# Kernel tuning notes

Measured on AMD Instinct MI355X. Metric: run time of the kernel, lower is better.

## Reference

```python
import jax, jax.numpy as jnp
import numpy as np

COORD_DIM = 2
ENTITY_DIM = 1024
FIELD_DIM = 512
INPUT_DIM = 512
NUM_ENTITIES = 512
FIELD_RESOLUTION = 10000  # grid_size = 100


def _gelu(x):
    return jax.nn.gelu(x, approximate=False)  # torch nn.GELU default (erf)


def setup_inputs() -> dict:
    key = jax.random.key(0)
    ks = jax.random.split(key, 9)
    std = 0.02  # matches _init_parameters
    B, S = 8, 4096
    x = jax.random.normal(ks[0], (B, S, INPUT_DIM), dtype=jnp.float32)
    # DensityField: density_projection = Linear(D,F) GELU Linear(F,F) GELU; coordinate_generator = Linear(F,2)
    W1 = jax.random.normal(ks[1], (INPUT_DIM, FIELD_DIM), jnp.float32) * std
    b1 = jnp.zeros((FIELD_DIM,), jnp.float32)
    W2 = jax.random.normal(ks[2], (FIELD_DIM, FIELD_DIM), jnp.float32) * std
    b2 = jnp.zeros((FIELD_DIM,), jnp.float32)
    Wc = jax.random.normal(ks[3], (FIELD_DIM, COORD_DIM), jnp.float32) * std
    bc = jnp.zeros((COORD_DIM,), jnp.float32)
    # entity_mapper: Linear(F+2, F) GELU Linear(F, E+2+1)
    We1 = jax.random.normal(ks[4], (FIELD_DIM + COORD_DIM, FIELD_DIM), jnp.float32) * std
    be1 = jnp.zeros((FIELD_DIM,), jnp.float32)
    We2 = jax.random.normal(ks[5], (FIELD_DIM, ENTITY_DIM + COORD_DIM + 1), jnp.float32) * std
    be2 = jnp.zeros((ENTITY_DIM + COORD_DIM + 1,), jnp.float32)
    # output_projection: Linear(E, 2E) GELU Linear(2E, D)
    Wo1 = jax.random.normal(ks[6], (ENTITY_DIM, 2 * ENTITY_DIM), jnp.float32) * std
    bo1 = jnp.zeros((2 * ENTITY_DIM,), jnp.float32)
    Wo2 = jax.random.normal(ks[7], (2 * ENTITY_DIM, INPUT_DIM), jnp.float32) * std
    bo2 = jnp.zeros((INPUT_DIM,), jnp.float32)
    return dict(x=x, W1=W1, b1=b1, W2=W2, b2=b2, Wc=Wc, bc=bc,
                We1=We1, be1=be1, We2=We2, be2=be2,
                Wo1=Wo1, bo1=bo1, Wo2=Wo2, bo2=bo2)


def _forward(x, W1, b1, W2, b2, Wc, bc, We1, be1, We2, be2, Wo1, bo1, Wo2, bo2):
    # --- DensityField ---
    df = _gelu(_gelu(x @ W1 + b1) @ W2 + b2)          # [B,S,F]
    coords = df @ Wc + bc                              # [B,S,2]
    # --- ContinuousEntityExtractor ---
    field_input = jnp.concatenate([coords, df], axis=-1)          # [B,S,2+F]
    ef = _gelu(field_input @ We1 + be1) @ We2 + be2                # [B,S,E+3]
    importance = jnp.linalg.norm(ef, axis=-1)                      # [B,S]
    _, top_idx = jax.lax.top_k(importance, NUM_ENTITIES)           # [B,Ne]
    sel = jnp.take_along_axis(ef, top_idx[..., None], axis=1)     # [B,Ne,E+3]
    positions = sel[..., :COORD_DIM]                               # [B,Ne,2]
    states = sel[..., COORD_DIM:COORD_DIM + ENTITY_DIM]            # [B,Ne,E]
    # --- ContinuousOutputGenerator ---
    proj = _gelu(states @ Wo1 + bo1) @ Wo2 + bo2                   # [B,Ne,D]
    grid_size = int(FIELD_RESOLUTION ** 0.5)
    g = jnp.linspace(-1.0, 1.0, grid_size)
    gx, gy = jnp.meshgrid(g, g, indexing='ij')
    grid = jnp.stack([gx.ravel(), gy.ravel()], axis=-1)            # [G2,2]
    # squared euclidean distances via expansion (torch: cdist then **2)
    g2 = jnp.sum(grid * grid, axis=-1)                             # [G2]
    p2 = jnp.sum(positions * positions, axis=-1)                   # [B,Ne]
    gp = jnp.einsum('gc,bnc->bgn', grid, positions)                # [B,G2,Ne]
    sq = g2[None, :, None] + p2[:, None, :] - 2.0 * gp             # [B,G2,Ne]
    attn = jnp.exp(-sq / 0.1)
    attn = attn / (attn.sum(axis=-1, keepdims=True) + 1e-8)
    out = jnp.einsum('bgn,bnd->bgd', attn, proj)                   # [B,G2,D]
    return out


def reference(x, W1, b1, W2, b2, Wc, bc, We1, be1, We2, be2, Wo1, bo1, Wo2, bo2):
    return _forward(x, W1, b1, W2, b2, Wc, bc, We1, be1, We2, be2, Wo1, bo1, Wo2, bo2)
```

## Files before the change

### kernel.cpp

```cpp
#include <hip/hip_runtime.h>
#include <hip/hip_bf16.h>
#include <math.h>


typedef __attribute__((ext_vector_type(8))) short bf16x8;
typedef __attribute__((ext_vector_type(4))) float f32x4;

__device__ __forceinline__ float gelu_exact(float x) {
    return 0.5f * x * (1.0f + erff(x * 0.7071067811865476f));
}

__device__ __forceinline__ void async_copy16(const void* g, void* l) {
    __builtin_amdgcn_global_load_lds(
        (const __attribute__((address_space(1))) unsigned int*)g,
        (__attribute__((address_space(3))) unsigned int*)l, 16, 0, 0);
}

__global__ __launch_bounds__(256) void split_kernel(
    const float* __restrict__ in,
    __hip_bfloat16* __restrict__ hi, __hip_bfloat16* __restrict__ lo)
{
    const int i4 = blockIdx.x * 256 + threadIdx.x;
    const float4 v = ((const float4*)in)[i4];
    __hip_bfloat16 h0 = __float2bfloat16(v.x);
    __hip_bfloat16 h1 = __float2bfloat16(v.y);
    __hip_bfloat16 h2 = __float2bfloat16(v.z);
    __hip_bfloat16 h3 = __float2bfloat16(v.w);
    __hip_bfloat16 l0 = __float2bfloat16(v.x - __bfloat162float(h0));
    __hip_bfloat16 l1 = __float2bfloat16(v.y - __bfloat162float(h1));
    __hip_bfloat16 l2 = __float2bfloat16(v.z - __bfloat162float(h2));
    __hip_bfloat16 l3 = __float2bfloat16(v.w - __bfloat162float(h3));
    union { __hip_bfloat16 h[4]; short4 s; } uh, ul;
    uh.h[0] = h0; uh.h[1] = h1; uh.h[2] = h2; uh.h[3] = h3;
    ul.h[0] = l0; ul.h[1] = l1; ul.h[2] = l2; ul.h[3] = l3;
    ((short4*)hi)[i4] = uh.s;
    ((short4*)lo)[i4] = ul.s;
}

__global__ __launch_bounds__(256) void transpose_split_kernel(
    const float* __restrict__ in,
    __hip_bfloat16* __restrict__ outH, __hip_bfloat16* __restrict__ outL,
    int K, int N)
{
    __shared__ float tile[32][33];
    const int k0 = blockIdx.y * 32, n0 = blockIdx.x * 32;
    const int t = threadIdx.x;
    const int lr = t >> 5, lc = t & 31;
    #pragma unroll
    for (int p = 0; p < 4; p++) {
        const int r = p * 8 + lr;
        const int n = n0 + lc;
        tile[r][lc] = (n < N) ? in[(size_t)(k0 + r) * N + n] : 0.f;
    }
    __syncthreads();
    #pragma unroll
    for (int p = 0; p < 4; p++) {
        const int r = p * 8 + lr;
        const float v = tile[lc][r];
        const __hip_bfloat16 h = __float2bfloat16(v);
        const __hip_bfloat16 l = __float2bfloat16(v - __bfloat162float(h));
        outH[(size_t)(n0 + r) * K + k0 + lc] = h;
        outL[(size_t)(n0 + r) * K + k0 + lc] = l;
    }
}

__global__ __launch_bounds__(256) void init_kernel(
    float* __restrict__ IMP, float* __restrict__ CRD,
    const float* __restrict__ bc)
{
    const int t = blockIdx.x * 256 + threadIdx.x;
    IMP[t] = 0.f;
    ((float2*)CRD)[t] = make_float2(bc[0], bc[1]);
}

template<bool GELU, bool RANK2, bool EFMODE, bool FUSEC>
__global__ __launch_bounds__(256, 2) void gemm3k(
    const __hip_bfloat16* __restrict__ Ahi, const __hip_bfloat16* __restrict__ Alo,
    const __hip_bfloat16* __restrict__ Bhi, const __hip_bfloat16* __restrict__ Blo,
    const float* __restrict__ bias,
    __hip_bfloat16* __restrict__ Chi, __hip_bfloat16* __restrict__ Clo,
    __hip_bfloat16* __restrict__ EFB, float* __restrict__ EFC,
    float* __restrict__ IMP,
    const float* __restrict__ A2, const float* __restrict__ W2r,
    float* __restrict__ CRD, const float* __restrict__ Wc)
{
    __shared__ __align__(16) __hip_bfloat16 AsH[2][4096];
    __shared__ __align__(16) __hip_bfloat16 AsL[2][4096];
    __shared__ __align__(16) __hip_bfloat16 BsH[2][4096];
    __shared__ __align__(16) __hip_bfloat16 BsL[2][4096];
    const int t = threadIdx.x;
    const int wave = t >> 6, lane = t & 63;
    const int wave_m = wave >> 1, wave_n = wave & 1;
    const int fr = lane & 15, quad = lane >> 4;
    const int gx = gridDim.x;
    const int nwg = gx * gridDim.y;
    int lid = blockIdx.y * gx + blockIdx.x;
    {
        const int chunk = nwg >> 3;
        lid = (lid & 7) * chunk + (lid >> 3);
    }
    const int m0 = (lid / gx) * 128;
    const int n0 = (lid % gx) * 128;
    const int lrow   = lane & 15;
    const int lchunk = (lane >> 4) * 8;

    f32x4 acc[4][4] = {};

    auto STAGE = [&](int buf, int step) {
        const int kk = step << 5;
        #pragma unroll
        for (int s = 0; s < 2; s++) {
            const int seg = wave * 2 + s;
            const size_t ao = (size_t)(m0 + seg * 16 + lrow) * 512 + kk + lchunk;
            const size_t bo = (size_t)(n0 + seg * 16 + lrow) * 512 + kk + lchunk;
            async_copy16(Ahi + ao, &AsH[buf][seg * 512]);
            async_copy16(Alo + ao, &AsL[buf][seg * 512]);
            async_copy16(Bhi + bo, &BsH[buf][seg * 512]);
            async_copy16(Blo + bo, &BsL[buf][seg * 512]);
        }
    };

    STAGE(0, 0);
    __syncthreads();
    int cur = 0;
    const int abase = wave_m * 2048 + quad * 128 + fr * 8;
    const int bbase = wave_n * 2048 + quad * 128 + fr * 8;
    for (int step = 0; step < 16; ++step) {
        if (step + 1 < 16) STAGE(cur ^ 1, step + 1);
        bf16x8 ah[4], al[4], bh[4], bl[4];
        #pragma unroll
        for (int i = 0; i < 4; i++) {
            ah[i] = *(const bf16x8*)&AsH[cur][abase + i * 512];
            al[i] = *(const bf16x8*)&AsL[cur][abase + i * 512];
        }
        #pragma unroll
        for (int j = 0; j < 4; j++) {
            bh[j] = *(const bf16x8*)&BsH[cur][bbase + j * 512];
            bl[j] = *(const bf16x8*)&BsL[cur][bbase + j * 512];
        }
        __builtin_amdgcn_s_setprio(1);
        #pragma unroll
        for (int i = 0; i < 4; i++)
            #pragma unroll
            for (int j = 0; j < 4; j++)
                acc[i][j] = __builtin_amdgcn_mfma_f32_16x16x32_bf16(
                    ah[i], bh[j], acc[i][j], 0, 0, 0);
        #pragma unroll
        for (int i = 0; i < 4; i++)
            #pragma unroll
            for (int j = 0; j < 4; j++)
                acc[i][j] = __builtin_amdgcn_mfma_f32_16x16x32_bf16(
                    ah[i], bl[j], acc[i][j], 0, 0, 0);
        #pragma unroll
        for (int i = 0; i < 4; i++)
            #pragma unroll
            for (int j = 0; j < 4; j++)
                acc[i][j] = __builtin_amdgcn_mfma_f32_16x16x32_bf16(
                    al[i], bh[j], acc[i][j], 0, 0, 0);
        __builtin_amdgcn_s_setprio(0);
        __syncthreads();
        cur ^= 1;
    }

    #pragma unroll
    for (int i = 0; i < 4; i++) {
        const int gmb = m0 + wave_m * 64 + i * 16 + quad * 4;
        float a2x[4], a2y[4];
        if (RANK2) {
            #pragma unroll
            for (int r = 0; r < 4; r++) {
                a2x[r] = A2[(size_t)(gmb + r) * 2];
                a2y[r] = A2[(size_t)(gmb + r) * 2 + 1];
            }
        }
        float f0[4] = {0.f, 0.f, 0.f, 0.f};
        float f1[4] = {0.f, 0.f, 0.f, 0.f};
        #pragma unroll
        for (int j = 0; j < 4; j++) {
            const int gn = n0 + wave_n * 64 + j * 16 + fr;
            const bool nok = !EFMODE || (gn < 1027);
            const float bv = nok ? bias[gn] : 0.f;
            float w2a = 0.f, w2b = 0.f;
            if (RANK2) { w2a = W2r[gn]; w2b = W2r[512 + gn]; }
            float wcx = 0.f, wcy = 0.f;
            if (FUSEC) {
                const float2 wc = ((const float2*)Wc)[gn];
                wcx = wc.x; wcy = wc.y;
            }
            #pragma unroll
            for (int r = 0; r < 4; r++) {
                const int gm = gmb + r;
                float v = acc[i][j][r] + bv;
                if (RANK2) v += a2x[r] * w2a + a2y[r] * w2b;
                if (GELU) v = gelu_exact(v);
                if (EFMODE) {
                    if (gn < 2) EFC[(size_t)gm * 2 + gn] = v;
                    else if (gn < 1026)
                        EFB[(size_t)gm * 1024 + gn - 2] = __float2bfloat16(v);
                    if (nok) f0[r] += v * v;
                } else {
                    const __hip_bfloat16 h = __float2bfloat16(v);
                    const __hip_bfloat16 l =
                        __float2bfloat16(v - __bfloat162float(h));
                    Chi[(size_t)gm * 512 + gn] = h;
                    Clo[(size_t)gm * 512 + gn] = l;
                    if (FUSEC) { f0[r] += v * wcx; f1[r] += v * wcy; }
                }
            }
        }
        if (EFMODE || FUSEC) {
            #pragma unroll
            for (int r = 0; r < 4; r++) {
                float a = f0[r], b = f1[r];
                #pragma unroll
                for (int off = 1; off < 16; off <<= 1) {
                    a += __shfl_xor(a, off);
                    if (FUSEC) b += __shfl_xor(b, off);
                }
                if (fr == 0) {
                    if (FUSEC) {
                        atomicAdd(&CRD[(size_t)(gmb + r) * 2],     a);
                        atomicAdd(&CRD[(size_t)(gmb + r) * 2 + 1], b);
                    } else {
                        atomicAdd(&IMP[gmb + r], a);
                    }
                }
            }
        }
    }
}

__global__ __launch_bounds__(1024) void topk_kernel(
    const float* __restrict__ IMP, int* __restrict__ IDX)
{
    __shared__ float v[4096];
    __shared__ int   ix[4096];
    const int b = blockIdx.x, t = threadIdx.x;
    for (int i = t; i < 4096; i += 1024) {
        v[i] = sqrtf(IMP[b * 4096 + i]);
        ix[i] = i;
    }
    __syncthreads();
    for (int k = 2; k <= 4096; k <<= 1) {
        for (int j = k >> 1; j > 0; j >>= 1) {
            for (int q = 0; q < 4; q++) {
                const int i = t + (q << 10);
                const int l = i ^ j;
                if (l > i) {
                    const float vi = v[i], vl = v[l];
                    const int   ii = ix[i], il = ix[l];
                    const bool after = (vi < vl) || (vi == vl && ii > il);
                    const bool dirAsc = ((i & k) == 0);
                    if (dirAsc ? after : !after) {
                        v[i] = vl; v[l] = vi; ix[i] = il; ix[l] = ii;
                    }
                }
            }
            __syncthreads();
        }
    }
    if (t < 512) IDX[b * 512 + t] = ix[t];
}

__global__ __launch_bounds__(256) void gather_kernel(
    const __hip_bfloat16* __restrict__ EFB, const float* __restrict__ EFC,
    const int* __restrict__ IDX,
    float* __restrict__ POS, __hip_bfloat16* __restrict__ ST)
{
    const int bn  = blockIdx.x;
    const int b   = bn >> 9;
    const int row = IDX[bn];
    const size_t src = (size_t)(b * 4096) + row;
    const int t = threadIdx.x;
    if (t < 2) POS[(size_t)bn * 2 + t] = EFC[src * 2 + t];
    const unsigned int* s = (const unsigned int*)(EFB + src * 1024);
    unsigned int* d = (unsigned int*)(ST + (size_t)bn * 1024);
    d[t]       = s[t];
    d[t + 256] = s[t + 256];
}

__global__ __launch_bounds__(256) void transpose_cvt_kernel(
    const float* __restrict__ in, __hip_bfloat16* __restrict__ out,
    int K, int N)
{
    __shared__ float tile[32][33];
    const int k0 = blockIdx.y * 32, n0 = blockIdx.x * 32;
    const int t = threadIdx.x;
    const int lr = t >> 5, lc = t & 31;
    #pragma unroll
    for (int p = 0; p < 4; p++) {
        const int r = p * 8 + lr;
        tile[r][lc] = in[(size_t)(k0 + r) * N + n0 + lc];
    }
    __syncthreads();
    #pragma unroll
    for (int p = 0; p < 4; p++) {
        const int r = p * 8 + lr;
        out[(size_t)(n0 + r) * K + k0 + lc] = __float2bfloat16(tile[lc][r]);
    }
}

__global__ __launch_bounds__(256) void transpose_proj_kernel(
    const __hip_bfloat16* __restrict__ in, __hip_bfloat16* __restrict__ out)
{
    __shared__ __hip_bfloat16 tile[32][33];
    const int b = blockIdx.z;
    const int n0 = blockIdx.y * 32, d0 = blockIdx.x * 32;
    const int t = threadIdx.x;
    const int lr = t >> 5, lc = t & 31;
    #pragma unroll
    for (int p = 0; p < 4; p++) {
        const int r = p * 8 + lr;
        tile[r][lc] = in[((size_t)b * 512 + n0 + r) * 512 + d0 + lc];
    }
    __syncthreads();
    #pragma unroll
    for (int p = 0; p < 4; p++) {
        const int r = p * 8 + lr;
        out[((size_t)b * 512 + d0 + r) * 512 + n0 + lc] = tile[lc][r];
    }
}

template<bool GELU>
__global__ __launch_bounds__(256, 4) void gemm_post(
    const __hip_bfloat16* __restrict__ A,
    const __hip_bfloat16* __restrict__ BT,
    const float* __restrict__ bias,
    __hip_bfloat16* __restrict__ C,
    int N, int K)
{
    __shared__ __align__(16) __hip_bfloat16 As[2][4096];
    __shared__ __align__(16) __hip_bfloat16 Bs[2][4096];
    const int t = threadIdx.x;
    const int wave = t >> 6, lane = t & 63;
    const int wave_m = wave >> 1, wave_n = wave & 1;
    const int fr = lane & 15, quad = lane >> 4;
    const int gx = gridDim.x;
    const int nwg = gx * gridDim.y;
    int lid = blockIdx.y * gx + blockIdx.x;
    {
        const int chunk = nwg >> 3;
        lid = (lid & 7) * chunk + (lid >> 3);
    }
    const int m0 = (lid / gx) * 128;
    const int n0 = (lid % gx) * 128;
    const int lrow   = lane & 15;
    const int lchunk = (lane >> 4) * 8;
    const int nsteps = K >> 5;

    f32x4 acc[4][4] = {};

    auto STAGE = [&](int buf, int step) {
        const int kk = step << 5;
        #pragma unroll
        for (int s = 0; s < 2; s++) {
            const int seg = wave * 2 + s;
            async_copy16(A  + (size_t)(m0 + seg * 16 + lrow) * K + kk + lchunk,
                         &As[buf][seg * 512]);
            async_copy16(BT + (size_t)(n0 + seg * 16 + lrow) * K + kk + lchunk,
                         &Bs[buf][seg * 512]);
        }
    };

    STAGE(0, 0);
    __syncthreads();
    int cur = 0;
    const int abase = wave_m * 2048 + quad * 128 + fr * 8;
    const int bbase = wave_n * 2048 + quad * 128 + fr * 8;
    for (int step = 0; step < nsteps; ++step) {
        if (step + 1 < nsteps) STAGE(cur ^ 1, step + 1);
        bf16x8 af[4], bfv[4];
        #pragma unroll
        for (int i = 0; i < 4; i++)
            af[i] = *(const bf16x8*)&As[cur][abase + i * 512];
        #pragma unroll
        for (int j = 0; j < 4; j++)
            bfv[j] = *(const bf16x8*)&Bs[cur][bbase + j * 512];
        __builtin_amdgcn_s_setprio(1);
        #pragma unroll
        for (int i = 0; i < 4; i++)
            #pragma unroll
            for (int j = 0; j < 4; j++)
                acc[i][j] = __builtin_amdgcn_mfma_f32_16x16x32_bf16(
                    af[i], bfv[j], acc[i][j], 0, 0, 0);
        __builtin_amdgcn_s_setprio(0);
        __syncthreads();
        cur ^= 1;
    }
    #pragma unroll
    for (int i = 0; i < 4; i++) {
        const int gm = m0 + wave_m * 64 + i * 16 + quad * 4;
        #pragma unroll
        for (int j = 0; j < 4; j++) {
            const int gn = n0 + wave_n * 64 + j * 16 + fr;
            const float bv = bias[gn];
            #pragma unroll
            for (int r = 0; r < 4; r++) {
                float v = acc[i][j][r] + bv;
                if (GELU) v = gelu_exact(v);
                C[(size_t)(gm + r) * N + gn] = __float2bfloat16(v);
            }
        }
    }
}

__global__ __launch_bounds__(256) void attn_mfma_kernel(
    const float* __restrict__ POS,
    const __hip_bfloat16* __restrict__ PROJT,
    float* __restrict__ OUT)
{
    __shared__ __align__(16) __hip_bfloat16 Bs[2][8192];
    __shared__ float2 pos_s[512];
    __shared__ float srow_s[4][16];
    const int t = threadIdx.x;
    const int wave = t >> 6, lane = t & 63;
    const int fr = lane & 15, quad = lane >> 4;
    const int b  = blockIdx.z;
    const int g0 = blockIdx.x * 64;
    const int d0 = blockIdx.y * 256;
    const int lrow   = lane & 15;
    const int lchunk = (lane >> 4) * 8;

    {
        const float2* p = (const float2*)(POS + (size_t)b * 512 * 2);
        pos_s[t]       = p[t];
        pos_s[256 + t] = p[256 + t];
    }
    const int g = g0 + wave * 16 + fr;
    const bool gv = g < 10000;
    const float step = 2.0f / 99.0f;
    const int gi = gv ? (g / 100) : 0;
    const int gj = gv ? (g - gi * 100) : 0;
    const float gx = -1.f + step * (float)gi;
    const float gy = -1.f + step * (float)gj;

    auto STAGE = [&](int buf, int n0s) {
        #pragma unroll
        for (int s = 0; s < 4; s++) {
            const int seg = wave * 4 + s;
            const __hip_bfloat16* gB = PROJT
                + ((size_t)b * 512 + d0 + seg * 16 + lrow) * 512
                + n0s + lchunk;
            async_copy16(gB, &Bs[buf][seg * 512]);
        }
    };

    f32x4 acc[16] = {};
    float wsum = 0.f;
    STAGE(0, 0);
    __syncthreads();
    int cur = 0;
    const int bbase = quad * 128 + fr * 8;

    for (int it = 0; it < 16; ++it) {
        const int n0 = it * 32;
        if (it + 1 < 16) STAGE(cur ^ 1, (it + 1) * 32);
        bf16x8 wf;
        float wl = 0.f;
        #pragma unroll
        for (int j = 0; j < 8; j++) {
            const int n = n0 + quad * 8 + j;
            const float2 pn = pos_s[n];
            const float dx = gx - pn.x, dy = gy - pn.y;
            const float w = gv ? __expf(-10.0f * (dx * dx + dy * dy)) : 0.f;
            const __hip_bfloat16 wb = __float2bfloat16(w);
            union { __hip_bfloat16 h; short s; } u; u.h = wb;
            wf[j] = u.s;
            wl += __bfloat162float(wb);
        }
        wsum += wl;
        __builtin_amdgcn_s_setprio(1);
        #pragma unroll
        for (int j = 0; j < 16; j++) {
            const bf16x8 bv = *(const bf16x8*)&Bs[cur][j * 512 + bbase];
            acc[j] = __builtin_amdgcn_mfma_f32_16x16x32_bf16(wf, bv, acc[j], 0, 0, 0);
        }
        __builtin_amdgcn_s_setprio(0);
        __syncthreads();
        cur ^= 1;
    }
    wsum += __shfl_xor(wsum, 16);
    wsum += __shfl_xor(wsum, 32);
    if (lane < 16) srow_s[wave][lane] = wsum;
    __syncthreads();
    const int rbase = quad * 4;
    float inv[4];
    #pragma unroll
    for (int r = 0; r < 4; r++)
        inv[r] = 1.0f / (srow_s[wave][rbase + r] + 1e-8f);
    #pragma unroll
    for (int j = 0; j < 16; j++) {
        const int col = d0 + j * 16 + fr;
        #pragma unroll
        for (int r = 0; r < 4; r++) {
            const int gr = g0 + wave * 16 + rbase + r;
            if (gr < 10000)
                OUT[((size_t)b * 10000 + gr) * 512 + col] = acc[j][r] * inv[r];
        }
    }
}

extern "C" void kernel_launch(void* const* d_in, const int* in_sizes, int n_in,
                              void* d_out, int out_size, void* d_ws, size_t ws_size,
                              hipStream_t stream)
{
    const float* x   = (const float*)d_in[0];
    const float* W1  = (const float*)d_in[1];
    const float* b1  = (const float*)d_in[2];
    const float* W2  = (const float*)d_in[3];
    const float* b2  = (const float*)d_in[4];
    const float* Wc  = (const float*)d_in[5];
    const float* bc  = (const float*)d_in[6];
    const float* We1 = (const float*)d_in[7];
    const float* be1 = (const float*)d_in[8];
    const float* We2 = (const float*)d_in[9];
    const float* be2 = (const float*)d_in[10];
    const float* Wo1 = (const float*)d_in[11];
    const float* bo1 = (const float*)d_in[12];
    const float* Wo2 = (const float*)d_in[13];
    const float* bo2 = (const float*)d_in[14];
    float* out = (float*)d_out;

    const size_t BS = 32768;
    const size_t ACT = BS * 512;
    __hip_bfloat16* P0h = (__hip_bfloat16*)d_ws;
    __hip_bfloat16* P0l = P0h + ACT;
    __hip_bfloat16* P1h = P0l + ACT;
    __hip_bfloat16* P1l = P1h + ACT;
    __hip_bfloat16* EFB = P1l + ACT;
    float* EFC = (float*)(EFB + BS * 1024);
    float* CRD = EFC + BS * 2;
    float* IMP = CRD + BS * 2;
    int*   IDX = (int*)(IMP + BS);
    float* POS = (float*)(IDX + 4096);
    __hip_bfloat16* W1Th = (__hip_bfloat16*)(POS + 4096 * 2);
    __hip_bfloat16* W1Tl = W1Th + 512 * 512;
    __hip_bfloat16* W2Th = W1Tl + 512 * 512;
    __hip_bfloat16* W2Tl = W2Th + 512 * 512;
    __hip_bfloat16* We1Th = W2Tl + 512 * 512;
    __hip_bfloat16* We1Tl = We1Th + 512 * 512;
    __hip_bfloat16* We2Th = We1Tl + 512 * 512;
    __hip_bfloat16* We2Tl = We2Th + (size_t)1152 * 512;
    __hip_bfloat16* ST    = P0h;
    __hip_bfloat16* H4    = ST + (size_t)4096 * 1024;
    __hip_bfloat16* PROJ  = H4 + (size_t)4096 * 2048;
    __hip_bfloat16* PROJT = PROJ + (size_t)4096 * 512;
    __hip_bfloat16* Wo1T  = PROJT + (size_t)4096 * 512;
    __hip_bfloat16* Wo2T  = Wo1T + (size_t)2048 * 1024;

    dim3 blk(256);
    split_kernel<<<dim3(16384), blk, 0, stream>>>(x, P0h, P0l);
    transpose_split_kernel<<<dim3(16, 16), blk, 0, stream>>>(W1, W1Th, W1Tl, 512, 512);
    transpose_split_kernel<<<dim3(16, 16), blk, 0, stream>>>(W2, W2Th, W2Tl, 512, 512);
    transpose_split_kernel<<<dim3(16, 16), blk, 0, stream>>>(We1 + 2 * 512, We1Th, We1Tl, 512, 512);
    transpose_split_kernel<<<dim3(36, 16), blk, 0, stream>>>(We2, We2Th, We2Tl, 512, 1027);
    init_kernel<<<dim3(128), blk, 0, stream>>>(IMP, CRD, bc);
    gemm3k<true, false, false, false><<<dim3(4, 256), blk, 0, stream>>>(
        P0h, P0l, W1Th, W1Tl, b1, P1h, P1l,
        nullptr, nullptr, nullptr, nullptr, nullptr, nullptr, nullptr);
    gemm3k<true, false, false, true><<<dim3(4, 256), blk, 0, stream>>>(
        P1h, P1l, W2Th, W2Tl, b2, P0h, P0l,
        nullptr, nullptr, nullptr, nullptr, nullptr, CRD, Wc);
    gemm3k<true, true, false, false><<<dim3(4, 256), blk, 0, stream>>>(
        P0h, P0l, We1Th, We1Tl, be1, P1h, P1l,
        nullptr, nullptr, nullptr, CRD, We1, nullptr, nullptr);
    gemm3k<false, false, true, false><<<dim3(9, 256), blk, 0, stream>>>(
        P1h, P1l, We2Th, We2Tl, be2, nullptr, nullptr,
        EFB, EFC, IMP, nullptr, nullptr, nullptr, nullptr);
    topk_kernel<<<dim3(8), dim3(1024), 0, stream>>>(IMP, IDX);
    transpose_cvt_kernel<<<dim3(64, 32), blk, 0, stream>>>(Wo1, Wo1T, 1024, 2048);
    transpose_cvt_kernel<<<dim3(16, 64), blk, 0, stream>>>(Wo2, Wo2T, 2048, 512);
    gather_kernel<<<dim3(4096), blk, 0, stream>>>(EFB, EFC, IDX, POS, ST);
    gemm_post<true><<<dim3(16, 32), blk, 0, stream>>>(
        ST, Wo1T, bo1, H4, 2048, 1024);
    gemm_post<false><<<dim3(4, 32), blk, 0, stream>>>(
        H4, Wo2T, bo2, PROJ, 512, 2048);
    transpose_proj_kernel<<<dim3(16, 16, 8), blk, 0, stream>>>(PROJ, PROJT);
    attn_mfma_kernel<<<dim3(157, 2, 8), blk, 0, stream>>>(POS, PROJT, out);
}
```

Baseline: 976.0 us.

## Load split-bf16 GEMM fragments directly from global and simplify LDS staging

The split-precision gemm3k drops LDS staging and instead loads MFMA fragments straight from global memory into registers. Two register sets are ping-ponged so the next K-step's loads are in flight while the current MFMAs run, and the XCD tile remapping is reworked. gemm_post and the attention kernel change their LDS layout to row-major [rows][32] with a different lane-to-address mapping and drop s_setprio. The attention kernel also goes from double to single buffering with an extra barrier. This trades LDS traffic and barriers for uncoalesced, cache-dependent global loads, and it loses the copy/compute overlap in the attention kernel.

```diff
diff --git a/kernel.cpp b/kernel.cpp
--- a/kernel.cpp
+++ b/kernel.cpp
@@ -84,83 +84,69 @@
     const float* __restrict__ A2, const float* __restrict__ W2r,
     float* __restrict__ CRD, const float* __restrict__ Wc)
 {
-    __shared__ __align__(16) __hip_bfloat16 AsH[2][4096];
-    __shared__ __align__(16) __hip_bfloat16 AsL[2][4096];
-    __shared__ __align__(16) __hip_bfloat16 BsH[2][4096];
-    __shared__ __align__(16) __hip_bfloat16 BsL[2][4096];
     const int t = threadIdx.x;
     const int wave = t >> 6, lane = t & 63;
     const int wave_m = wave >> 1, wave_n = wave & 1;
     const int fr = lane & 15, quad = lane >> 4;
     const int gx = gridDim.x;
-    const int nwg = gx * gridDim.y;
-    int lid = blockIdx.y * gx + blockIdx.x;
-    {
-        const int chunk = nwg >> 3;
-        lid = (lid & 7) * chunk + (lid >> 3);
-    }
-    const int m0 = (lid / gx) * 128;
-    const int n0 = (lid % gx) * 128;
-    const int lrow   = lane & 15;
-    const int lchunk = (lane >> 4) * 8;
+    const int L = blockIdx.y * gx + blockIdx.x;
+    const int xcd = L & 7, kk_ = L >> 3;
+    const int m_blk = xcd * (gridDim.y >> 3) + kk_ / gx;
+    const int n_blk = kk_ % gx;
+    const int m0 = m_blk * 128;
+    const int n0 = n_blk * 128;
+
+    const __hip_bfloat16* pAh = Ahi + (size_t)(m0 + wave_m * 64 + fr) * 512 + quad * 8;
+    const __hip_bfloat16* pAl = Alo + (size_t)(m0 + wave_m * 64 + fr) * 512 + quad * 8;
+    const __hip_bfloat16* pBh = Bhi + (size_t)(n0 + wave_n * 64 + fr) * 512 + quad * 8;
+    const __hip_bfloat16* pBl = Blo + (size_t)(n0 + wave_n * 64 + fr) * 512 + quad * 8;
 
     f32x4 acc[4][4] = {};
 
-    auto STAGE = [&](int buf, int step) {
-        const int kk = step << 5;
-        #pragma unroll
-        for (int s = 0; s < 2; s++) {
-            const int seg = wave * 2 + s;
-            const size_t ao = (size_t)(m0 + seg * 16 + lrow) * 512 + kk + lchunk;
-            const size_t bo = (size_t)(n0 + seg * 16 + lrow) * 512 + kk + lchunk;
-            async_copy16(Ahi + ao, &AsH[buf][seg * 512]);
-            async_copy16(Alo + ao, &AsL[buf][seg * 512]);
-            async_copy16(Bhi + bo, &BsH[buf][seg * 512]);
-            async_copy16(Blo + bo, &BsL[buf][seg * 512]);
-        }
-    };
-
-    STAGE(0, 0);
-    __syncthreads();
-    int cur = 0;
-    const int abase = wave_m * 2048 + quad * 128 + fr * 8;
-    const int bbase = wave_n * 2048 + quad * 128 + fr * 8;
-    for (int step = 0; step < 16; ++step) {
-        if (step + 1 < 16) STAGE(cur ^ 1, step + 1);
-        bf16x8 ah[4], al[4], bh[4], bl[4];
-        #pragma unroll
-        for (int i = 0; i < 4; i++) {
-            ah[i] = *(const bf16x8*)&AsH[cur][abase + i * 512];
-            al[i] = *(const bf16x8*)&AsL[cur][abase + i * 512];
-        }
-        #pragma unroll
-        for (int j = 0; j < 4; j++) {
-            bh[j] = *(const bf16x8*)&BsH[cur][bbase + j * 512];
-            bl[j] = *(const bf16x8*)&BsL[cur][bbase + j * 512];
-        }
-        __builtin_amdgcn_s_setprio(1);
-        #pragma unroll
-        for (int i = 0; i < 4; i++)
-            #pragma unroll
-            for (int j = 0; j < 4; j++)
-                acc[i][j] = __builtin_amdgcn_mfma_f32_16x16x32_bf16(
-                    ah[i], bh[j], acc[i][j], 0, 0, 0);
-        #pragma unroll
-        for (int i = 0; i < 4; i++)
-            #pragma unroll
-            for (int j = 0; j < 4; j++)
-                acc[i][j] = __builtin_amdgcn_mfma_f32_16x16x32_bf16(
-                    ah[i], bl[j], acc[i][j], 0, 0, 0);
-        #pragma unroll
-        for (int i = 0; i < 4; i++)
-            #pragma unroll
-            for (int j = 0; j < 4; j++)
-                acc[i][j] = __builtin_amdgcn_mfma_f32_16x16x32_bf16(
-                    al[i], bh[j], acc[i][j], 0, 0, 0);
-        __builtin_amdgcn_s_setprio(0);
-        __syncthreads();
-        cur ^= 1;
-    }
+    struct FragSet { bf16x8 ah[4], al[4], bh[4], bl[4]; };
+    FragSet s0, s1;
+
+#define LOAD_SET(S, KK) do {                                              \
+        _Pragma("unroll")                                                 \
+        for (int i_ = 0; i_ < 4; i_++) {                                  \
+            S.ah[i_] = *(const bf16x8*)(pAh + (size_t)i_ * 8192 + (KK));  \
+            S.al[i_] = *(const bf16x8*)(pAl + (size_t)i_ * 8192 + (KK));  \
+            S.bh[i_] = *(const bf16x8*)(pBh + (size_t)i_ * 8192 + (KK));  \
+            S.bl[i_] = *(const bf16x8*)(pBl + (size_t)i_ * 8192 + (KK));  \
+        }                                                                 \
+    } while (0)
+
+#define MFMA_SET(S) do {                                                  \
+        _Pragma("unroll")                                                 \
+        for (int i_ = 0; i_ < 4; i_++)                                    \
+            _Pragma("unroll")                                             \
+            for (int j_ = 0; j_ < 4; j_++)                                \
+                acc[i_][j_] = __builtin_amdgcn_mfma_f32_16x16x32_bf16(    \
+                    S.ah[i_], S.bh[j_], acc[i_][j_], 0, 0, 0);            \
+        _Pragma("unroll")                                                 \
+        for (int i_ = 0; i_ < 4; i_++)                                    \
+            _Pragma("unroll")                                             \
+            for (int j_ = 0; j_ < 4; j_++)                                \
+                acc[i_][j_] = __builtin_amdgcn_mfma_f32_16x16x32_bf16(    \
+                    S.ah[i_], S.bl[j_], acc[i_][j_], 0, 0, 0);            \
+        _Pragma("unroll")                                                 \
+        for (int i_ = 0; i_ < 4; i_++)                                    \
+            _Pragma("unroll")                                             \
+            for (int j_ = 0; j_ < 4; j_++)                                \
+                acc[i_][j_] = __builtin_amdgcn_mfma_f32_16x16x32_bf16(    \
+                    S.al[i_], S.bh[j_], acc[i_][j_], 0, 0, 0);            \
+    } while (0)
+
+    LOAD_SET(s0, 0);
+    for (int step = 0; step < 16; step += 2) {
+        LOAD_SET(s1, (step + 1) << 5);
+        MFMA_SET(s0);
+        const int kn = ((step + 2 < 16) ? (step + 2) : 15) << 5;
+        LOAD_SET(s0, kn);
+        MFMA_SET(s1);
+    }
+#undef LOAD_SET
+#undef MFMA_SET
 
     #pragma unroll
     for (int i = 0; i < 4; i++) {
@@ -329,8 +315,8 @@
     __hip_bfloat16* __restrict__ C,
     int N, int K)
 {
-    __shared__ __align__(16) __hip_bfloat16 As[2][4096];
-    __shared__ __align__(16) __hip_bfloat16 Bs[2][4096];
+    __shared__ __align__(16) __hip_bfloat16 As[2][128][32];
+    __shared__ __align__(16) __hip_bfloat16 Bs[2][128][32];
     const int t = threadIdx.x;
     const int wave = t >> 6, lane = t & 63;
     const int wave_m = wave >> 1, wave_n = wave & 1;
@@ -344,8 +330,8 @@
     }
     const int m0 = (lid / gx) * 128;
     const int n0 = (lid % gx) * 128;
-    const int lrow   = lane & 15;
-    const int lchunk = (lane >> 4) * 8;
+    const int srow = lane >> 2;
+    const int skc  = (lane & 3) * 8;
     const int nsteps = K >> 5;
 
     f32x4 acc[4][4] = {};
@@ -355,35 +341,32 @@
         #pragma unroll
         for (int s = 0; s < 2; s++) {
             const int seg = wave * 2 + s;
-            async_copy16(A  + (size_t)(m0 + seg * 16 + lrow) * K + kk + lchunk,
-                         &As[buf][seg * 512]);
-            async_copy16(BT + (size_t)(n0 + seg * 16 + lrow) * K + kk + lchunk,
-                         &Bs[buf][seg * 512]);
+            const int row = seg * 16 + srow;
+            async_copy16(A  + (size_t)(m0 + row) * K + kk + skc,
+                         &As[buf][seg * 16][0]);
+            async_copy16(BT + (size_t)(n0 + row) * K + kk + skc,
+                         &Bs[buf][seg * 16][0]);
         }
     };
 
     STAGE(0, 0);
     __syncthreads();
     int cur = 0;
-    const int abase = wave_m * 2048 + quad * 128 + fr * 8;
-    const int bbase = wave_n * 2048 + quad * 128 + fr * 8;
     for (int step = 0; step < nsteps; ++step) {
         if (step + 1 < nsteps) STAGE(cur ^ 1, step + 1);
         bf16x8 af[4], bfv[4];
         #pragma unroll
         for (int i = 0; i < 4; i++)
-            af[i] = *(const bf16x8*)&As[cur][abase + i * 512];
+            af[i] = *(const bf16x8*)&As[cur][wave_m * 64 + i * 16 + fr][quad * 8];
         #pragma unroll
         for (int j = 0; j < 4; j++)
-            bfv[j] = *(const bf16x8*)&Bs[cur][bbase + j * 512];
-        __builtin_amdgcn_s_setprio(1);
+            bfv[j] = *(const bf16x8*)&Bs[cur][wave_n * 64 + j * 16 + fr][quad * 8];
         #pragma unroll
         for (int i = 0; i < 4; i++)
             #pragma unroll
             for (int j = 0; j < 4; j++)
                 acc[i][j] = __builtin_amdgcn_mfma_f32_16x16x32_bf16(
                     af[i], bfv[j], acc[i][j], 0, 0, 0);
-        __builtin_amdgcn_s_setprio(0);
         __syncthreads();
         cur ^= 1;
     }
@@ -409,7 +392,7 @@
     const __hip_bfloat16* __restrict__ PROJT,
     float* __restrict__ OUT)
 {
-    __shared__ __align__(16) __hip_bfloat16 Bs[2][8192];
+    __shared__ __align__(16) __hip_bfloat16 Bs[256][32];
     __shared__ float2 pos_s[512];
     __shared__ float srow_s[4][16];
     const int t = threadIdx.x;
@@ -418,8 +401,6 @@
     const int b  = blockIdx.z;
     const int g0 = blockIdx.x * 64;
     const int d0 = blockIdx.y * 256;
-    const int lrow   = lane & 15;
-    const int lchunk = (lane >> 4) * 8;
 
     {
         const float2* p = (const float2*)(POS + (size_t)b * 512 * 2);
@@ -434,27 +415,19 @@
     const float gx = -1.f + step * (float)gi;
     const float gy = -1.f + step * (float)gj;
 
-    auto STAGE = [&](int buf, int n0s) {
+    f32x4 acc[16] = {};
+    float wsum = 0.f;
+    __syncthreads();
+
+    for (int n0 = 0; n0 < 512; n0 += 32) {
         #pragma unroll
         for (int s = 0; s < 4; s++) {
             const int seg = wave * 4 + s;
             const __hip_bfloat16* gB = PROJT
-                + ((size_t)b * 512 + d0 + seg * 16 + lrow) * 512
-                + n0s + lchunk;
-            async_copy16(gB, &Bs[buf][seg * 512]);
-        }
-    };
-
-    f32x4 acc[16] = {};
-    float wsum = 0.f;
-    STAGE(0, 0);
-    __syncthreads();
-    int cur = 0;
-    const int bbase = quad * 128 + fr * 8;
-
-    for (int it = 0; it < 16; ++it) {
-        const int n0 = it * 32;
-        if (it + 1 < 16) STAGE(cur ^ 1, (it + 1) * 32);
+                + ((size_t)b * 512 + d0 + seg * 16 + (lane >> 2)) * 512
+                + n0 + (lane & 3) * 8;
+            async_copy16(gB, &Bs[seg * 16][0]);
+        }
         bf16x8 wf;
         float wl = 0.f;
         #pragma unroll
@@ -469,15 +442,13 @@
             wl += __bfloat162float(wb);
         }
         wsum += wl;
-        __builtin_amdgcn_s_setprio(1);
+        __syncthreads();
         #pragma unroll
         for (int j = 0; j < 16; j++) {
-            const bf16x8 bv = *(const bf16x8*)&Bs[cur][j * 512 + bbase];
+            const bf16x8 bv = *(const bf16x8*)&Bs[j * 16 + fr][quad * 8];
             acc[j] = __builtin_amdgcn_mfma_f32_16x16x32_bf16(wf, bv, acc[j], 0, 0, 0);
         }
-        __builtin_amdgcn_s_setprio(0);
         __syncthreads();
-        cur ^= 1;
     }
     wsum += __shfl_xor(wsum, 16);
     wsum += __shfl_xor(wsum, 32);
```

New measurement: 1.224 ms. +25.4%, slower.
